# Kernel optimization log

Hardware: AMD Instinct MI355X
Metric: run time of the kernel (lower is better)

The kernel has to match this reference:

```python
import jax, jax.numpy as jnp
import numpy as np

B, S, D, H = 2, 2048, 768, 12
HD = D // H


def setup_inputs() -> dict:
    key = jax.random.key(0)
    ks = jax.random.split(key, 8)
    scale = 1.0 / np.sqrt(D)
    inp = {
        "q": jax.random.normal(ks[0], (B, S, D), jnp.float32),
        "k": jax.random.normal(ks[1], (B, S, D), jnp.float32),
        "v": jax.random.normal(ks[2], (B, S, D), jnp.float32),
        # causal mask: 1.0 where attention is disallowed (upper triangle)
        "mask": jnp.triu(jnp.ones((S, S), jnp.float32), k=1)[None, None, :, :],
        "Wq": jax.random.normal(ks[3], (D, D), jnp.float32) * scale,
        "bq": jnp.zeros((D,), jnp.float32),
        "Wk": jax.random.normal(ks[4], (D, D), jnp.float32) * scale,
        "bk": jnp.zeros((D,), jnp.float32),
        "Wv": jax.random.normal(ks[5], (D, D), jnp.float32) * scale,
        "bv": jnp.zeros((D,), jnp.float32),
        "Wo": jax.random.normal(ks[6], (D, D), jnp.float32) * scale,
        "bo": jnp.zeros((D,), jnp.float32),
    }
    return inp


def _split_heads(x):
    # [B, S, D] -> [B, H, S, HD]
    b, s, _ = x.shape
    return x.reshape(b, s, H, HD).transpose(0, 2, 1, 3)


def reference(q, k, v, mask, Wq, bq, Wk, bk, Wv, bv, Wo, bo):
    qh = _split_heads(q @ Wq + bq)
    kh = _split_heads(k @ Wk + bk)
    vh = _split_heads(v @ Wv + bv)
    scale = 1.0 / jnp.sqrt(jnp.asarray(HD, qh.dtype))
    # [B, H, Sq, Sk] — full attention matrix, as in the original
    scores = jnp.einsum("bhqd,bhkd->bhqk", qh, kh) * scale
    scores = scores + mask * -1e9
    attn = jax.nn.softmax(scores, axis=-1)  # dropout is identity at inference
    out = jnp.einsum("bhqk,bhkd->bhqd", attn, vh)
    out = out.transpose(0, 2, 1, 3).reshape(q.shape[0], -1, D)
    return out @ Wo + bo
```

## Files before the change

### kernel.cpp

```cpp
#include <hip/hip_runtime.h>

#define SEQ    2048
#define NB     2
#define DMODEL 768
#define NH     12
#define HDIM   64
#define BS     (NB * SEQ)

typedef __bf16  bf16x8  __attribute__((ext_vector_type(8)));
typedef ushort  ushort8 __attribute__((ext_vector_type(8)));
typedef float   floatx4 __attribute__((ext_vector_type(4)));

#define GLOBAL_AS __attribute__((address_space(1)))
#define LDS_AS    __attribute__((address_space(3)))

union PackU8 { ushort u[8]; uint4 v; };
union PackU4 { ushort u[4]; uint2 v; };

__device__ __forceinline__ ushort f2bf(float x) {
    union { float f; unsigned u; } t; t.f = x;
    unsigned r = t.u + 0x7fffu + ((t.u >> 16) & 1u);
    return (ushort)(r >> 16);
}

__device__ __forceinline__ bf16x8 ld_frag(const ushort* p) {
    return __builtin_bit_cast(bf16x8, *(const ushort8*)p);
}

__global__ void convert_x(const float* __restrict__ q, const float* __restrict__ k,
                          const float* __restrict__ v,
                          ushort* __restrict__ qo, ushort* __restrict__ ko,
                          ushort* __restrict__ vo)
{
    const float* src = blockIdx.z == 0 ? q : blockIdx.z == 1 ? k : v;
    ushort*      dst = blockIdx.z == 0 ? qo : blockIdx.z == 1 ? ko : vo;
    const int i = (blockIdx.x * 256 + threadIdx.x) * 4;
    const float4 f = *(const float4*)(src + i);
    ushort4 o;
    o.x = f2bf(f.x); o.y = f2bf(f.y); o.z = f2bf(f.z); o.w = f2bf(f.w);
    *(ushort4*)(dst + i) = o;
}

__global__ __launch_bounds__(256)
void convert_wT(const float* __restrict__ wq, const float* __restrict__ wk,
                const float* __restrict__ wv, const float* __restrict__ wo,
                ushort* __restrict__ wtcat, ushort* __restrict__ wto)
{
    __shared__ float Tf[64][69];
    const int z = blockIdx.z;
    const float* w = z == 0 ? wq : z == 1 ? wk : z == 2 ? wv : wo;
    ushort*      o = z < 3 ? wtcat + (size_t)z * DMODEL * DMODEL : wto;
    const int k0 = blockIdx.x * 64, n0 = blockIdx.y * 64;
    const int tid = threadIdx.x;
#pragma unroll
    for (int p = 0; p < 4; ++p) {
        const int idx = tid + p * 256;
        const int r = idx >> 4, c = (idx & 15) * 4;
        const float4 f = *(const float4*)&w[(size_t)(k0 + r) * DMODEL + n0 + c];
        Tf[r][c] = f.x; Tf[r][c + 1] = f.y; Tf[r][c + 2] = f.z; Tf[r][c + 3] = f.w;
    }
    __syncthreads();
#pragma unroll
    for (int p = 0; p < 2; ++p) {
        const int idx = tid + p * 256;
        const int n = idx >> 3, kk = (idx & 7) * 8;
        PackU8 pk;
#pragma unroll
        for (int j = 0; j < 8; ++j) pk.u[j] = f2bf(Tf[kk + j][n]);
        *(uint4*)&o[(size_t)(n0 + n) * DMODEL + k0 + kk] = pk.v;
    }
}

__global__ __launch_bounds__(256)
void gemm_qkv(const ushort* __restrict__ xq, const ushort* __restrict__ xk,
              const ushort* __restrict__ xv, const ushort* __restrict__ WT,
              const float* __restrict__ bq, const float* __restrict__ bk,
              const float* __restrict__ bv,
              ushort* __restrict__ oq, ushort* __restrict__ ok,
              ushort* __restrict__ ov)
{
    __shared__ __align__(16) ushort As[128 * 32];
    __shared__ __align__(16) ushort Bs[128 * 32];

    const int z = blockIdx.y / 6;
    const ushort* X = z == 0 ? xq : z == 1 ? xk : xv;

    const int tid  = threadIdx.x;
    const int lane = tid & 63;
    const int w    = tid >> 6;
    const int l15  = lane & 15;
    const int quad = lane >> 4;
    const int wm   = (w >> 1) * 64;
    const int wn   = (w & 1) * 64;
    const int row0 = blockIdx.x * 128;
    const int col0 = blockIdx.y * 128;

    floatx4 acc[4][4];
    const floatx4 fzero = {0.f, 0.f, 0.f, 0.f};
#pragma unroll
    for (int i = 0; i < 4; ++i)
#pragma unroll
        for (int j = 0; j < 4; ++j) acc[i][j] = fzero;

    const int rin = lane >> 2;
    const int gc  = (lane & 3) * 8;

    for (int k0 = 0; k0 < DMODEL; k0 += 32) {
#pragma unroll
        for (int p = 0; p < 2; ++p) {
            const int ch = w * 2 + p;
            const int r  = ch * 16 + rin;
            __builtin_amdgcn_global_load_lds(
                (const GLOBAL_AS uint*)&X[(size_t)(row0 + r) * DMODEL + k0 + gc],
                (LDS_AS uint*)&As[ch * 512], 16, 0, 0);
            __builtin_amdgcn_global_load_lds(
                (const GLOBAL_AS uint*)&WT[(size_t)(col0 + r) * DMODEL + k0 + gc],
                (LDS_AS uint*)&Bs[ch * 512], 16, 0, 0);
        }
        __syncthreads();

        bf16x8 af[4], bfr[4];
#pragma unroll
        for (int t = 0; t < 4; ++t) {
            af[t]  = ld_frag(&As[(wm + t * 16 + l15) * 32 + quad * 8]);
            bfr[t] = ld_frag(&Bs[(wn + t * 16 + l15) * 32 + quad * 8]);
        }
#pragma unroll
        for (int ti = 0; ti < 4; ++ti)
#pragma unroll
            for (int tj = 0; tj < 4; ++tj)
                acc[ti][tj] = __builtin_amdgcn_mfma_f32_16x16x32_bf16(
                    af[ti], bfr[tj], acc[ti][tj], 0, 0, 0);
        __syncthreads();
    }

    const int c0 = (blockIdx.y % 6) * 128;
    const float*  bias = z == 0 ? bq : z == 1 ? bk : bv;
    ushort*       out  = z == 0 ? oq : z == 1 ? ok : ov;
#pragma unroll
    for (int tj = 0; tj < 4; ++tj) {
        const int c_l = c0 + wn + tj * 16 + l15;
        const float bb = bias[c_l];
        const int h  = c_l >> 6;
        const int dd = c_l & 63;
#pragma unroll
        for (int ti = 0; ti < 4; ++ti) {
#pragma unroll
            for (int ri = 0; ri < 4; ++ri) {
                const int r_g = row0 + wm + ti * 16 + quad * 4 + ri;
                const int b   = r_g >> 11;
                const int s   = r_g & (SEQ - 1);
                out[(((size_t)(b * NH + h) * SEQ + s) << 6) + dd] =
                    f2bf(acc[ti][tj][ri] + bb);
            }
        }
    }
}

__global__ __launch_bounds__(256)
void gemm_out(const ushort* __restrict__ X, const ushort* __restrict__ WT,
              const float* __restrict__ bias, float* __restrict__ fo)
{
    __shared__ __align__(16) ushort As[64][40];
    __shared__ __align__(16) ushort Bs[128][40];

    const int tid  = threadIdx.x;
    const int lane = tid & 63;
    const int wv   = tid >> 6;
    const int wm   = (wv >> 1) * 32;
    const int wn   = (wv & 1) * 64;
    const int l15  = lane & 15;
    const int quad = lane >> 4;
    const int row0 = blockIdx.x * 64;
    const int col0 = blockIdx.y * 128;

    floatx4 acc[2][4];
    const floatx4 fzero = {0.f, 0.f, 0.f, 0.f};
#pragma unroll
    for (int i = 0; i < 2; ++i)
#pragma unroll
        for (int j = 0; j < 4; ++j) acc[i][j] = fzero;

    const int sr = tid >> 2;
    const int sc = (tid & 3) * 8;

    for (int k0 = 0; k0 < DMODEL; k0 += 32) {
        *(uint4*)&As[sr][sc] = *(const uint4*)&X[(size_t)(row0 + sr) * DMODEL + k0 + sc];
#pragma unroll
        for (int p = 0; p < 2; ++p) {
            const int r = sr + p * 64;
            *(uint4*)&Bs[r][sc] = *(const uint4*)&WT[(size_t)(col0 + r) * DMODEL + k0 + sc];
        }
        __syncthreads();

        bf16x8 af[2], bfr[4];
#pragma unroll
        for (int t = 0; t < 2; ++t)
            af[t] = ld_frag(&As[wm + t * 16 + l15][quad * 8]);
#pragma unroll
        for (int t = 0; t < 4; ++t)
            bfr[t] = ld_frag(&Bs[wn + t * 16 + l15][quad * 8]);
#pragma unroll
        for (int ti = 0; ti < 2; ++ti)
#pragma unroll
            for (int tj = 0; tj < 4; ++tj)
                acc[ti][tj] = __builtin_amdgcn_mfma_f32_16x16x32_bf16(
                    af[ti], bfr[tj], acc[ti][tj], 0, 0, 0);
        __syncthreads();
    }

#pragma unroll
    for (int tj = 0; tj < 4; ++tj) {
        const int c_g = col0 + wn + tj * 16 + l15;
        const float bb = bias[c_g];
#pragma unroll
        for (int ti = 0; ti < 2; ++ti)
#pragma unroll
            for (int ri = 0; ri < 4; ++ri) {
                const int r_g = row0 + wm + ti * 16 + quad * 4 + ri;
                fo[(size_t)r_g * DMODEL + c_g] = acc[ti][tj][ri] + bb;
            }
    }
}

__global__ void transpose_v(const ushort* __restrict__ vh, ushort* __restrict__ vt)
{
    __shared__ __align__(16) ushort T[64][72];
    const int bh = blockIdx.y;
    const int s0 = blockIdx.x * 64;
    const ushort* src = vh + (size_t)bh * SEQ * HDIM;
    ushort*       dst = vt + (size_t)bh * HDIM * SEQ;

#pragma unroll
    for (int p = 0; p < 2; ++p) {
        const int idx = threadIdx.x + p * 256;
        const int r = idx >> 3, c = (idx & 7) * 8;
        *(uint4*)&T[r][c] = *(const uint4*)&src[(size_t)(s0 + r) * HDIM + c];
    }
    __syncthreads();
#pragma unroll
    for (int p = 0; p < 2; ++p) {
        const int idx = threadIdx.x + p * 256;
        const int d = idx >> 3, c = (idx & 7) * 8;
        PackU8 pk;
#pragma unroll
        for (int j = 0; j < 8; ++j) pk.u[j] = T[c + j][d];
        *(uint4*)&dst[(size_t)d * SEQ + s0 + c] = pk.v;
    }
}

#define APAD 88

__device__ __forceinline__ void attn_epilogue(ushort* __restrict__ ctx, int b, int h,
                                              int qtile, int wv, int quad, int l15,
                                              const floatx4* O, float l)
{
    const float inv = 1.f / l;
    float ib[4];
#pragma unroll
    for (int ri = 0; ri < 4; ++ri) ib[ri] = __shfl(inv, quad * 4 + ri);
#pragma unroll
    for (int dj = 0; dj < 4; ++dj)
#pragma unroll
        for (int ri = 0; ri < 4; ++ri) {
            const int row = qtile * 32 + wv * 16 + quad * 4 + ri;
            ctx[((size_t)b * SEQ + row) * DMODEL + h * HDIM + dj * 16 + l15] =
                f2bf(O[dj][ri] * ib[ri]);
        }
}

__global__ __launch_bounds__(128)
void attn_mfma(const ushort* __restrict__ qh, const ushort* __restrict__ kh,
               const ushort* __restrict__ vt, ushort* __restrict__ ctx)
{
    __shared__ __align__(16) ushort Ks[2][64][APAD];
    __shared__ __align__(16) ushort Vs[2][64][APAD];
    __shared__ __align__(16) ushort Ps[32][APAD];

    const int tid  = threadIdx.x;
    const int lane = tid & 63;
    const int wv   = tid >> 6;
    const int l15  = lane & 15;
    const int quad = lane >> 4;
    const int id  = blockIdx.x;
    const int xcd = id & 7;
    const int jj  = id >> 3;
    const int g   = jj >> 5;
    const int x   = jj & 31;
    const int bh  = xcd + 8 * g;
    const int b   = bh / NH, h = bh - b * NH;
    const int qA  = x, qB = 63 - x;
    const int nkA = (qA >> 1) + 1;
    const size_t base = (size_t)bh * SEQ * HDIM;

    const float SCL = 0.125f * 1.44269504f;

    bf16x8 qfA[2], qfB[2];
#pragma unroll
    for (int ks = 0; ks < 2; ++ks) {
        qfA[ks] = ld_frag(&qh[base + (size_t)(qA * 32 + wv * 16 + l15) * HDIM + ks * 32 + quad * 8]);
        qfB[ks] = ld_frag(&qh[base + (size_t)(qB * 32 + wv * 16 + l15) * HDIM + ks * 32 + quad * 8]);
    }

    const int sr = tid >> 3;
    const int sc = (tid & 7) * 8;

    uint4 kreg[4], vreg[4];
#pragma unroll
    for (int p = 0; p < 4; ++p) {
        const int r = sr + p * 16;
        kreg[p] = *(const uint4*)&kh[base + (size_t)r * HDIM + sc];
        vreg[p] = *(const uint4*)&vt[base + (size_t)r * SEQ + sc];
    }
#pragma unroll
    for (int p = 0; p < 4; ++p) {
        const int r = sr + p * 16;
        *(uint4*)&Ks[0][r][sc] = kreg[p];
        *(uint4*)&Vs[0][r][sc] = vreg[p];
    }

    float l = 0.f;
    floatx4 O[4];
    const floatx4 fzero = {0.f, 0.f, 0.f, 0.f};
#pragma unroll
    for (int dj = 0; dj < 4; ++dj) O[dj] = fzero;

    const int rowA = qA * 32 + wv * 16 + l15;
    const int rowB = qB * 32 + wv * 16 + l15;

    for (int t = 0; t <= 32; ++t) {
        __syncthreads();
        const int buf = t & 1;

        if (t < 32) {
            const int kn  = (t + 1 < nkA) ? (t + 1) : (t + 1 - nkA);
            const int c0n = kn * 64;
#pragma unroll
            for (int p = 0; p < 4; ++p) {
                const int r = sr + p * 16;
                kreg[p] = *(const uint4*)&kh[base + (size_t)(c0n + r) * HDIM + sc];
                vreg[p] = *(const uint4*)&vt[base + (size_t)r * SEQ + c0n + sc];
            }
        }

        const bool isA   = (t < nkA);
        const int  kt    = isA ? t : t - nkA;
        const int  c0    = kt * 64;
        const bool diag  = (t == nkA - 1) || (t == 32);
        const int  row_g = isA ? rowA : rowB;

        floatx4 S[4];
#pragma unroll
        for (int nj = 0; nj < 4; ++nj) {
            S[nj] = fzero;
#pragma unroll
            for (int ks = 0; ks < 2; ++ks) {
                const bf16x8 kf = ld_frag(&Ks[buf][nj * 16 + l15][ks * 32 + quad * 8]);
                const bf16x8 qf = isA ? qfA[ks] : qfB[ks];
                S[nj] = __builtin_amdgcn_mfma_f32_16x16x32_bf16(kf, qf, S[nj], 0, 0, 0);
            }
        }

        float rs = 0.f;
#pragma unroll
        for (int nj = 0; nj < 4; ++nj) {
            PackU4 pk;
#pragma unroll
            for (int ri = 0; ri < 4; ++ri) {
                float p = __builtin_amdgcn_exp2f(S[nj][ri] * SCL);
                if (diag && (c0 + nj * 16 + quad * 4 + ri > row_g)) p = 0.f;
                rs += p;
                union { float f; unsigned u; } tb; tb.f = p;
                pk.u[ri] = (ushort)(tb.u >> 16);
            }
            *(uint2*)&Ps[wv * 16 + l15][nj * 16 + quad * 4] = pk.v;
        }
        rs += __shfl_xor(rs, 16);
        rs += __shfl_xor(rs, 32);
        l += rs;

        bf16x8 pf[2];
#pragma unroll
        for (int ks = 0; ks < 2; ++ks)
            pf[ks] = ld_frag(&Ps[wv * 16 + l15][ks * 32 + quad * 8]);
#pragma unroll
        for (int dj = 0; dj < 4; ++dj)
#pragma unroll
            for (int ks = 0; ks < 2; ++ks) {
                const bf16x8 vfr = ld_frag(&Vs[buf][dj * 16 + l15][ks * 32 + quad * 8]);
                O[dj] = __builtin_amdgcn_mfma_f32_16x16x32_bf16(pf[ks], vfr, O[dj], 0, 0, 0);
            }

        if (t == nkA - 1) {
            attn_epilogue(ctx, b, h, qA, wv, quad, l15, O, l);
            l = 0.f;
#pragma unroll
            for (int dj = 0; dj < 4; ++dj) O[dj] = fzero;
        }

        if (t < 32) {
#pragma unroll
            for (int p = 0; p < 4; ++p) {
                const int r = sr + p * 16;
                *(uint4*)&Ks[buf ^ 1][r][sc] = kreg[p];
                *(uint4*)&Vs[buf ^ 1][r][sc] = vreg[p];
            }
        }
    }

    attn_epilogue(ctx, b, h, qB, wv, quad, l15, O, l);
}

extern "C" void kernel_launch(void* const* d_in, const int* in_sizes, int n_in,
                              void* d_out, int out_size, void* d_ws, size_t ws_size,
                              hipStream_t stream)
{
    const float* q  = (const float*)d_in[0];
    const float* k  = (const float*)d_in[1];
    const float* v  = (const float*)d_in[2];
    const float* Wq = (const float*)d_in[4];
    const float* bq = (const float*)d_in[5];
    const float* Wk = (const float*)d_in[6];
    const float* bk = (const float*)d_in[7];
    const float* Wv = (const float*)d_in[8];
    const float* bv = (const float*)d_in[9];
    const float* Wo = (const float*)d_in[10];
    const float* bo = (const float*)d_in[11];
    float* out = (float*)d_out;

    char* ws = (char*)d_ws;
    const size_t ACT = (size_t)BS * DMODEL * 2;
    ushort* qx    = (ushort*)(ws);
    ushort* kx    = (ushort*)(ws + ACT);
    ushort* vx    = (ushort*)(ws + 2 * ACT);
    ushort* qhp   = (ushort*)(ws + 3 * ACT);
    ushort* khp   = (ushort*)(ws + 4 * ACT);
    ushort* vhp   = (ushort*)(ws + 5 * ACT);
    ushort* wtcat = (ushort*)(ws + 6 * ACT);
    ushort* wto   = wtcat + (size_t)3 * DMODEL * DMODEL;
    ushort* vhT   = vx;
    ushort* ctx   = qx;

    convert_x<<<dim3(BS * DMODEL / 1024, 1, 3), 256, 0, stream>>>(q, k, v, qx, kx, vx);
    convert_wT<<<dim3(12, 12, 4), 256, 0, stream>>>(Wq, Wk, Wv, Wo, wtcat, wto);
    gemm_qkv<<<dim3(BS / 128, 18), 256, 0, stream>>>(
        qx, kx, vx, wtcat, bq, bk, bv, qhp, khp, vhp);
    transpose_v<<<dim3(SEQ / 64, NB * NH), 256, 0, stream>>>(vhp, vhT);
    attn_mfma<<<dim3(768), 128, 0, stream>>>(qhp, khp, vhT, ctx);
    gemm_out<<<dim3(BS / 64, DMODEL / 128), 256, 0, stream>>>(ctx, wto, bo, out);
}
```

Baseline: 207.7 us.

## Fuse fp32-to-bf16 input conversion into QKV GEMM and restructure attention split

Removes the separate convert_x kernel: the QKV GEMM now loads fp32 activations directly and packs them to bf16 (truncating via byte permute) into LDS. The attention kernel drops LDS staging of K/V, reading fragments directly from global memory. Each wave now handles half the keys for all 32 query rows, and partial outputs and row sums are combined through LDS in the epilogue. P packing uses truncation with a swizzled LDS layout. This trades an extra kernel and LDS double-buffering for more global/L2 fragment loads and a cross-wave reduction, and input rounding changes from round-to-nearest to truncation.

```diff
diff --git a/kernel.cpp b/kernel.cpp
--- a/kernel.cpp
+++ b/kernel.cpp
@@ -15,7 +15,6 @@
 #define LDS_AS    __attribute__((address_space(3)))
 
 union PackU8 { ushort u[8]; uint4 v; };
-union PackU4 { ushort u[4]; uint2 v; };
 
 __device__ __forceinline__ ushort f2bf(float x) {
     union { float f; unsigned u; } t; t.f = x;
@@ -23,22 +22,13 @@
     return (ushort)(r >> 16);
 }
 
+__device__ __forceinline__ unsigned bfpack(float hi, float lo) {
+    union { float f; unsigned u; } a, b; a.f = hi; b.f = lo;
+    return __builtin_amdgcn_perm(a.u, b.u, 0x07060302u);
+}
+
 __device__ __forceinline__ bf16x8 ld_frag(const ushort* p) {
     return __builtin_bit_cast(bf16x8, *(const ushort8*)p);
-}
-
-__global__ void convert_x(const float* __restrict__ q, const float* __restrict__ k,
-                          const float* __restrict__ v,
-                          ushort* __restrict__ qo, ushort* __restrict__ ko,
-                          ushort* __restrict__ vo)
-{
-    const float* src = blockIdx.z == 0 ? q : blockIdx.z == 1 ? k : v;
-    ushort*      dst = blockIdx.z == 0 ? qo : blockIdx.z == 1 ? ko : vo;
-    const int i = (blockIdx.x * 256 + threadIdx.x) * 4;
-    const float4 f = *(const float4*)(src + i);
-    ushort4 o;
-    o.x = f2bf(f.x); o.y = f2bf(f.y); o.z = f2bf(f.z); o.w = f2bf(f.w);
-    *(ushort4*)(dst + i) = o;
 }
 
 __global__ __launch_bounds__(256)
@@ -72,8 +62,8 @@
 }
 
 __global__ __launch_bounds__(256)
-void gemm_qkv(const ushort* __restrict__ xq, const ushort* __restrict__ xk,
-              const ushort* __restrict__ xv, const ushort* __restrict__ WT,
+void gemm_qkv(const float* __restrict__ xq, const float* __restrict__ xk,
+              const float* __restrict__ xv, const ushort* __restrict__ WT,
               const float* __restrict__ bq, const float* __restrict__ bk,
               const float* __restrict__ bv,
               ushort* __restrict__ oq, ushort* __restrict__ ok,
@@ -83,7 +73,7 @@
     __shared__ __align__(16) ushort Bs[128 * 32];
 
     const int z = blockIdx.y / 6;
-    const ushort* X = z == 0 ? xq : z == 1 ? xk : xv;
+    const float* X = z == 0 ? xq : z == 1 ? xk : xv;
 
     const int tid  = threadIdx.x;
     const int lane = tid & 63;
@@ -104,6 +94,8 @@
 
     const int rin = lane >> 2;
     const int gc  = (lane & 3) * 8;
+    const int xr  = tid >> 1;
+    const int xc  = (tid & 1) * 16;
 
     for (int k0 = 0; k0 < DMODEL; k0 += 32) {
 #pragma unroll
@@ -111,11 +103,22 @@
             const int ch = w * 2 + p;
             const int r  = ch * 16 + rin;
             __builtin_amdgcn_global_load_lds(
-                (const GLOBAL_AS uint*)&X[(size_t)(row0 + r) * DMODEL + k0 + gc],
-                (LDS_AS uint*)&As[ch * 512], 16, 0, 0);
-            __builtin_amdgcn_global_load_lds(
                 (const GLOBAL_AS uint*)&WT[(size_t)(col0 + r) * DMODEL + k0 + gc],
                 (LDS_AS uint*)&Bs[ch * 512], 16, 0, 0);
+        }
+        {
+            const float* Xr = X + (size_t)(row0 + xr) * DMODEL + k0 + xc;
+            const float4 a0 = *(const float4*)(Xr);
+            const float4 a1 = *(const float4*)(Xr + 4);
+            const float4 a2 = *(const float4*)(Xr + 8);
+            const float4 a3 = *(const float4*)(Xr + 12);
+            uint4 w0, w1;
+            w0.x = bfpack(a0.y, a0.x); w0.y = bfpack(a0.w, a0.z);
+            w0.z = bfpack(a1.y, a1.x); w0.w = bfpack(a1.w, a1.z);
+            w1.x = bfpack(a2.y, a2.x); w1.y = bfpack(a2.w, a2.z);
+            w1.z = bfpack(a3.y, a3.x); w1.w = bfpack(a3.w, a3.z);
+            *(uint4*)&As[xr * 32 + xc]     = w0;
+            *(uint4*)&As[xr * 32 + xc + 8] = w1;
         }
         __syncthreads();
 
@@ -249,37 +252,17 @@
     }
 }
 
-#define APAD 88
-
-__device__ __forceinline__ void attn_epilogue(ushort* __restrict__ ctx, int b, int h,
-                                              int qtile, int wv, int quad, int l15,
-                                              const floatx4* O, float l)
-{
-    const float inv = 1.f / l;
-    float ib[4];
-#pragma unroll
-    for (int ri = 0; ri < 4; ++ri) ib[ri] = __shfl(inv, quad * 4 + ri);
-#pragma unroll
-    for (int dj = 0; dj < 4; ++dj)
-#pragma unroll
-        for (int ri = 0; ri < 4; ++ri) {
-            const int row = qtile * 32 + wv * 16 + quad * 4 + ri;
-            ctx[((size_t)b * SEQ + row) * DMODEL + h * HDIM + dj * 16 + l15] =
-                f2bf(O[dj][ri] * ib[ri]);
-        }
-}
-
 __global__ __launch_bounds__(128)
 void attn_mfma(const ushort* __restrict__ qh, const ushort* __restrict__ kh,
                const ushort* __restrict__ vt, ushort* __restrict__ ctx)
 {
-    __shared__ __align__(16) ushort Ks[2][64][APAD];
-    __shared__ __align__(16) ushort Vs[2][64][APAD];
-    __shared__ __align__(16) ushort Ps[32][APAD];
+    __shared__ __align__(16) ushort  Ps[2][32][32];
+    __shared__ __align__(16) floatx4 OB[2][2][2][64];
+    __shared__ float Lb[2][2][16];
 
     const int tid  = threadIdx.x;
     const int lane = tid & 63;
-    const int wv   = tid >> 6;
+    const int w    = tid >> 6;
     const int l15  = lane & 15;
     const int quad = lane >> 4;
     const int id  = blockIdx.x;
@@ -295,120 +278,148 @@
 
     const float SCL = 0.125f * 1.44269504f;
 
-    bf16x8 qfA[2], qfB[2];
-#pragma unroll
-    for (int ks = 0; ks < 2; ++ks) {
-        qfA[ks] = ld_frag(&qh[base + (size_t)(qA * 32 + wv * 16 + l15) * HDIM + ks * 32 + quad * 8]);
-        qfB[ks] = ld_frag(&qh[base + (size_t)(qB * 32 + wv * 16 + l15) * HDIM + ks * 32 + quad * 8]);
-    }
-
-    const int sr = tid >> 3;
-    const int sc = (tid & 7) * 8;
-
-    uint4 kreg[4], vreg[4];
-#pragma unroll
-    for (int p = 0; p < 4; ++p) {
-        const int r = sr + p * 16;
-        kreg[p] = *(const uint4*)&kh[base + (size_t)r * HDIM + sc];
-        vreg[p] = *(const uint4*)&vt[base + (size_t)r * SEQ + sc];
-    }
-#pragma unroll
-    for (int p = 0; p < 4; ++p) {
-        const int r = sr + p * 16;
-        *(uint4*)&Ks[0][r][sc] = kreg[p];
-        *(uint4*)&Vs[0][r][sc] = vreg[p];
-    }
-
-    float l = 0.f;
-    floatx4 O[4];
+    unsigned koff[2][2], voff[4];
+#pragma unroll
+    for (int nj = 0; nj < 2; ++nj)
+#pragma unroll
+        for (int ks = 0; ks < 2; ++ks)
+            koff[nj][ks] = (unsigned)(w * 32 + nj * 16 + l15) * HDIM + ks * 32 + quad * 8;
+#pragma unroll
+    for (int dj = 0; dj < 4; ++dj)
+        voff[dj] = (unsigned)(dj * 16 + l15) * SEQ + w * 32 + quad * 8;
+
+    bf16x8 qf[2][2];
+#pragma unroll
+    for (int qt = 0; qt < 2; ++qt)
+#pragma unroll
+        for (int ks = 0; ks < 2; ++ks)
+            qf[qt][ks] = ld_frag(&qh[base + (size_t)(qA * 32 + qt * 16 + l15) * HDIM
+                                      + ks * 32 + quad * 8]);
+
+    float lp[2] = {0.f, 0.f};
+    floatx4 O[2][4];
     const floatx4 fzero = {0.f, 0.f, 0.f, 0.f};
 #pragma unroll
-    for (int dj = 0; dj < 4; ++dj) O[dj] = fzero;
-
-    const int rowA = qA * 32 + wv * 16 + l15;
-    const int rowB = qB * 32 + wv * 16 + l15;
+    for (int mt = 0; mt < 2; ++mt)
+#pragma unroll
+        for (int dj = 0; dj < 4; ++dj) O[mt][dj] = fzero;
+
+    auto epilogue = [&](int qtile) {
+        float l0 = lp[0]; l0 += __shfl_xor(l0, 16); l0 += __shfl_xor(l0, 32);
+        float l1 = lp[1]; l1 += __shfl_xor(l1, 16); l1 += __shfl_xor(l1, 32);
+        if (quad == 0) { Lb[w][0][l15] = l0; Lb[w][1][l15] = l1; }
+#pragma unroll
+        for (int mt = 0; mt < 2; ++mt)
+#pragma unroll
+            for (int js = 0; js < 2; ++js)
+                OB[w][mt][js][lane] = O[mt][w == 0 ? 2 + js : js];
+        __syncthreads();
+#pragma unroll
+        for (int mt = 0; mt < 2; ++mt) {
+            const floatx4 la = *(const floatx4*)&Lb[0][mt][quad * 4];
+            const floatx4 lb = *(const floatx4*)&Lb[1][mt][quad * 4];
+            floatx4 inv;
+#pragma unroll
+            for (int ri = 0; ri < 4; ++ri) inv[ri] = 1.f / (la[ri] + lb[ri]);
+#pragma unroll
+            for (int js = 0; js < 2; ++js) {
+                const int dj = (w == 0) ? js : 2 + js;
+                const floatx4 om = O[mt][dj] + OB[w ^ 1][mt][js][lane];
+                const int col = h * HDIM + dj * 16 + l15;
+#pragma unroll
+                for (int ri = 0; ri < 4; ++ri) {
+                    const int row = qtile * 32 + mt * 16 + quad * 4 + ri;
+                    ctx[((size_t)b * SEQ + row) * DMODEL + col] = f2bf(om[ri] * inv[ri]);
+                }
+            }
+        }
+        __syncthreads();
+    };
 
     for (int t = 0; t <= 32; ++t) {
-        __syncthreads();
-        const int buf = t & 1;
-
-        if (t < 32) {
-            const int kn  = (t + 1 < nkA) ? (t + 1) : (t + 1 - nkA);
-            const int c0n = kn * 64;
-#pragma unroll
-            for (int p = 0; p < 4; ++p) {
-                const int r = sr + p * 16;
-                kreg[p] = *(const uint4*)&kh[base + (size_t)(c0n + r) * HDIM + sc];
-                vreg[p] = *(const uint4*)&vt[base + (size_t)r * SEQ + c0n + sc];
+        const bool isA = (t < nkA);
+        const int  kt  = isA ? t : t - nkA;
+        const int  c0  = kt * 64;
+        const bool diag = (t == nkA - 1) || (t == 32);
+        const int  qb0  = (isA ? qA : qB) * 32;
+        const unsigned cK = (unsigned)c0 * HDIM;
+
+        bf16x8 kf[2][2], vf[4];
+#pragma unroll
+        for (int nj = 0; nj < 2; ++nj)
+#pragma unroll
+            for (int ks = 0; ks < 2; ++ks)
+                kf[nj][ks] = ld_frag(&kh[base + cK + koff[nj][ks]]);
+#pragma unroll
+        for (int dj = 0; dj < 4; ++dj)
+            vf[dj] = ld_frag(&vt[base + (unsigned)c0 + voff[dj]]);
+
+        floatx4 S[2][2];
+#pragma unroll
+        for (int nj = 0; nj < 2; ++nj)
+#pragma unroll
+            for (int qt = 0; qt < 2; ++qt) {
+                S[nj][qt] = fzero;
+#pragma unroll
+                for (int ks = 0; ks < 2; ++ks)
+                    S[nj][qt] = __builtin_amdgcn_mfma_f32_16x16x32_bf16(
+                        kf[nj][ks], qf[qt][ks], S[nj][qt], 0, 0, 0);
             }
-        }
-
-        const bool isA   = (t < nkA);
-        const int  kt    = isA ? t : t - nkA;
-        const int  c0    = kt * 64;
-        const bool diag  = (t == nkA - 1) || (t == 32);
-        const int  row_g = isA ? rowA : rowB;
-
-        floatx4 S[4];
-#pragma unroll
-        for (int nj = 0; nj < 4; ++nj) {
-            S[nj] = fzero;
-#pragma unroll
-            for (int ks = 0; ks < 2; ++ks) {
-                const bf16x8 kf = ld_frag(&Ks[buf][nj * 16 + l15][ks * 32 + quad * 8]);
-                const bf16x8 qf = isA ? qfA[ks] : qfB[ks];
-                S[nj] = __builtin_amdgcn_mfma_f32_16x16x32_bf16(kf, qf, S[nj], 0, 0, 0);
+
+#pragma unroll
+        for (int qt = 0; qt < 2; ++qt) {
+            const int qrow = qb0 + qt * 16 + l15;
+#pragma unroll
+            for (int nj = 0; nj < 2; ++nj) {
+                float p[4];
+#pragma unroll
+                for (int ri = 0; ri < 4; ++ri)
+                    p[ri] = __builtin_amdgcn_exp2f(S[nj][qt][ri] * SCL);
+                if (diag) {
+#pragma unroll
+                    for (int ri = 0; ri < 4; ++ri)
+                        if (c0 + w * 32 + nj * 16 + quad * 4 + ri > qrow) p[ri] = 0.f;
+                }
+                lp[qt] += (p[0] + p[1]) + (p[2] + p[3]);
+                uint2 pk;
+                pk.x = bfpack(p[1], p[0]);
+                pk.y = bfpack(p[3], p[2]);
+                const int row    = qt * 16 + l15;
+                const int chunkx = (nj * 2 + (quad >> 1)) ^ (l15 & 3);
+                *(uint2*)&Ps[w][row][chunkx * 8 + (quad & 1) * 4] = pk;
             }
         }
 
-        float rs = 0.f;
-#pragma unroll
-        for (int nj = 0; nj < 4; ++nj) {
-            PackU4 pk;
-#pragma unroll
-            for (int ri = 0; ri < 4; ++ri) {
-                float p = __builtin_amdgcn_exp2f(S[nj][ri] * SCL);
-                if (diag && (c0 + nj * 16 + quad * 4 + ri > row_g)) p = 0.f;
-                rs += p;
-                union { float f; unsigned u; } tb; tb.f = p;
-                pk.u[ri] = (ushort)(tb.u >> 16);
-            }
-            *(uint2*)&Ps[wv * 16 + l15][nj * 16 + quad * 4] = pk.v;
-        }
-        rs += __shfl_xor(rs, 16);
-        rs += __shfl_xor(rs, 32);
-        l += rs;
-
         bf16x8 pf[2];
 #pragma unroll
-        for (int ks = 0; ks < 2; ++ks)
-            pf[ks] = ld_frag(&Ps[wv * 16 + l15][ks * 32 + quad * 8]);
-#pragma unroll
-        for (int dj = 0; dj < 4; ++dj)
-#pragma unroll
-            for (int ks = 0; ks < 2; ++ks) {
-                const bf16x8 vfr = ld_frag(&Vs[buf][dj * 16 + l15][ks * 32 + quad * 8]);
-                O[dj] = __builtin_amdgcn_mfma_f32_16x16x32_bf16(pf[ks], vfr, O[dj], 0, 0, 0);
-            }
+        for (int mt = 0; mt < 2; ++mt) {
+            const int chunkx = quad ^ (l15 & 3);
+            pf[mt] = ld_frag(&Ps[w][mt * 16 + l15][chunkx * 8]);
+        }
+#pragma unroll
+        for (int mt = 0; mt < 2; ++mt)
+#pragma unroll
+            for (int dj = 0; dj < 4; ++dj)
+                O[mt][dj] = __builtin_amdgcn_mfma_f32_16x16x32_bf16(
+                    pf[mt], vf[dj], O[mt][dj], 0, 0, 0);
 
         if (t == nkA - 1) {
-            attn_epilogue(ctx, b, h, qA, wv, quad, l15, O, l);
-            l = 0.f;
-#pragma unroll
-            for (int dj = 0; dj < 4; ++dj) O[dj] = fzero;
-        }
-
-        if (t < 32) {
-#pragma unroll
-            for (int p = 0; p < 4; ++p) {
-                const int r = sr + p * 16;
-                *(uint4*)&Ks[buf ^ 1][r][sc] = kreg[p];
-                *(uint4*)&Vs[buf ^ 1][r][sc] = vreg[p];
-            }
-        }
-    }
-
-    attn_epilogue(ctx, b, h, qB, wv, quad, l15, O, l);
+            epilogue(qA);
+            lp[0] = lp[1] = 0.f;
+#pragma unroll
+            for (int mt = 0; mt < 2; ++mt)
+#pragma unroll
+                for (int dj = 0; dj < 4; ++dj) O[mt][dj] = fzero;
+#pragma unroll
+            for (int qt = 0; qt < 2; ++qt)
+#pragma unroll
+                for (int ks = 0; ks < 2; ++ks)
+                    qf[qt][ks] = ld_frag(&qh[base + (size_t)(qB * 32 + qt * 16 + l15) * HDIM
+                                              + ks * 32 + quad * 8]);
+        }
+    }
+
+    epilogue(qB);
 }
 
 extern "C" void kernel_launch(void* const* d_in, const int* in_sizes, int n_in,
@@ -430,21 +441,17 @@
 
     char* ws = (char*)d_ws;
     const size_t ACT = (size_t)BS * DMODEL * 2;
-    ushort* qx    = (ushort*)(ws);
-    ushort* kx    = (ushort*)(ws + ACT);
-    ushort* vx    = (ushort*)(ws + 2 * ACT);
-    ushort* qhp   = (ushort*)(ws + 3 * ACT);
-    ushort* khp   = (ushort*)(ws + 4 * ACT);
-    ushort* vhp   = (ushort*)(ws + 5 * ACT);
-    ushort* wtcat = (ushort*)(ws + 6 * ACT);
+    ushort* qhp   = (ushort*)(ws);
+    ushort* khp   = (ushort*)(ws + ACT);
+    ushort* vhp   = (ushort*)(ws + 2 * ACT);
+    ushort* vhT   = (ushort*)(ws + 3 * ACT);
+    ushort* ctx   = (ushort*)(ws + 4 * ACT);
+    ushort* wtcat = (ushort*)(ws + 5 * ACT);
     ushort* wto   = wtcat + (size_t)3 * DMODEL * DMODEL;
-    ushort* vhT   = vx;
-    ushort* ctx   = qx;
-
-    convert_x<<<dim3(BS * DMODEL / 1024, 1, 3), 256, 0, stream>>>(q, k, v, qx, kx, vx);
+
     convert_wT<<<dim3(12, 12, 4), 256, 0, stream>>>(Wq, Wk, Wv, Wo, wtcat, wto);
     gemm_qkv<<<dim3(BS / 128, 18), 256, 0, stream>>>(
-        qx, kx, vx, wtcat, bq, bk, bv, qhp, khp, vhp);
+        q, k, v, wtcat, bq, bk, bv, qhp, khp, vhp);
     transpose_v<<<dim3(SEQ / 64, NB * NH), 256, 0, stream>>>(vhp, vhT);
     attn_mfma<<<dim3(768), 128, 0, stream>>>(qhp, khp, vhT, ctx);
     gemm_out<<<dim3(BS / 64, DMODEL / 128), 256, 0, stream>>>(ctx, wto, bo, out);
```

After: 217.5 us. 4.7% more time.
